# Performance work log

Measured on AMD Instinct MI355X. Metric: run time of the kernel, lower is better.

Reference implementation:

```python
import jax, jax.numpy as jnp
import numpy as np

K = 1024  # codebook size
D = 256   # embedding dim


def setup_inputs() -> dict:
    key = jax.random.key(0)
    k1, k2 = jax.random.split(key)
    z_e_x = jax.random.normal(k1, (32, D, 32, 32), dtype=jnp.float32)  # NCHW
    # nn.Embedding weight initialized uniform(-1/K, 1/K)
    W = jax.random.uniform(k2, (K, D), dtype=jnp.float32, minval=-1.0 / K, maxval=1.0 / K)
    return {"z_e_x": z_e_x, "W": W}


def reference(z_e_x, W):
    # permute NCHW -> NHWC, flatten spatial, nearest-codebook lookup (vq)
    z = jnp.transpose(z_e_x, (0, 2, 3, 1))            # [B, H, Wd, D]
    B, H, Wd, Dd = z.shape
    flat = z.reshape(-1, Dd)                           # [N, D]
    # squared L2 distances: ||z||^2 - 2 z.W^T + ||W||^2
    z_sq = jnp.sum(flat * flat, axis=1, keepdims=True)         # [N, 1]
    w_sq = jnp.sum(W * W, axis=1)                               # [K]
    dists = z_sq - 2.0 * (flat @ W.T) + w_sq[None, :]           # [N, K]
    idx = jnp.argmin(dists, axis=1)                             # [N]
    latents = idx.reshape(B, H, Wd)                             # [B, H, Wd] int indices
    return latents
```

## Files before the change

### kernel.cpp

```cpp
#include <hip/hip_runtime.h>

#define NPOS 32768
#define DDIM 256
#define KCODES 1024

typedef __attribute__((ext_vector_type(8))) short bf16x8;
typedef __attribute__((ext_vector_type(4))) float f32x4;
typedef unsigned long long u64;

__device__ __forceinline__ float sqr_rn(float x) {
    float r = x * x;
    asm volatile("" : "+v"(r));
    return r;
}
__device__ __forceinline__ float add_rn(float a, float b) {
    float r = a + b;
    asm volatile("" : "+v"(r));
    return r;
}

__device__ __forceinline__ unsigned short f2bf(float x) {
    unsigned u = __float_as_uint(x);
    return (unsigned short)((u + 0x7fffu + ((u >> 16) & 1u)) >> 16);
}

__device__ __forceinline__ u64 packm(float s, int code) {
    unsigned b = __float_as_uint(s);
    unsigned mm = ((unsigned)((int)b >> 31)) | 0x80000000u;
    return ((u64)(b ^ mm) << 32) | (unsigned)code;
}

__global__ __launch_bounds__(256) void wprep(const float* __restrict__ W,
                                             float* __restrict__ wsq,
                                             unsigned short* __restrict__ wb16t) {
    const int t   = threadIdx.x;
    const int bid = blockIdx.x;
    const int row = bid * 16 + (t >> 4);
    const int j   = t & 15;
    const float* base = W + row * DDIM + (j & 7) + (j >> 3) * 128;
    float r = sqr_rn(base[0]);
#pragma unroll
    for (int i = 1; i < 16; ++i) r = add_rn(r, sqr_rn(base[i * 8]));
#pragma unroll
    for (int m = 1; m <= 8; m <<= 1) r = add_rn(r, __shfl_xor(r, m));
    if (j == 0) wsq[row] = r;
#pragma unroll
    for (int jj = 0; jj < 2; ++jj) {
        const int u  = t + jj * 256;
        const int n  = bid * 16 + (u >> 5);
        const int k8 = u & 31;
        const float4 f0 = *(const float4*)&W[n * DDIM + k8 * 8];
        const float4 f1 = *(const float4*)&W[n * DDIM + k8 * 8 + 4];
        bf16x8 o;
        o[0] = (short)f2bf(f0.x); o[1] = (short)f2bf(f0.y);
        o[2] = (short)f2bf(f0.z); o[3] = (short)f2bf(f0.w);
        o[4] = (short)f2bf(f1.x); o[5] = (short)f2bf(f1.y);
        o[6] = (short)f2bf(f1.z); o[7] = (short)f2bf(f1.w);
        const int kk = k8 >> 2, kq = k8 & 3;
        *(bf16x8*)&wb16t[(n >> 8) * 65536 + kk * 8192 + kq * 2048 + (n & 255) * 8] = o;
    }
}

#define ZS 260
__global__ __launch_bounds__(256)
void vq_fused(const float* __restrict__ z,
              const float* __restrict__ W,
              const float* __restrict__ wsq,
              const unsigned short* __restrict__ wb16t,
              int* __restrict__ out) {
    union Sm {
        unsigned short At[8192];
        float          Zs[32 * ZS];
    };
    __shared__ Sm  sm;
    __shared__ u64 redL[32 * 8];

    const int t   = threadIdx.x;
    const int bid = blockIdx.x;
    const int img = bid >> 5;
    const int p0  = (bid & 31) * 32;

    {
        const float* zbase = z + img * (DDIM * 1024) + p0;
#pragma unroll
        for (int jj = 0; jj < 4; ++jj) {
            const int u_ = t + jj * 256;
            const int m  = u_ & 31;
            const int k8 = u_ >> 5;
            const float* src = zbase + k8 * 8192 + m;
            bf16x8 o;
#pragma unroll
            for (int e = 0; e < 8; ++e) o[e] = (short)f2bf(src[e * 1024]);
            *(bf16x8*)&sm.At[k8 * 256 + m * 8] = o;
        }
    }
    __syncthreads();

    const int w  = t >> 6;
    const int l  = t & 63;
    const int ln = l & 15;
    const int q  = l >> 4;
    const int nw = w * 64;

    const char* aBase = (const char*)sm.At + q * 512 + ln * 16;
    const char* bBase = (const char*)wb16t + q * 4096 + (nw + ln) * 16;

    float s0[2][4], s1[2][4];
    int   i0[2][4], i1[2][4];
#pragma unroll
    for (int mf = 0; mf < 2; ++mf)
#pragma unroll
        for (int reg = 0; reg < 4; ++reg) {
            s0[mf][reg] = 1e30f; s1[mf][reg] = 1e30f;
            i0[mf][reg] = 0;     i1[mf][reg] = 0;
        }

#pragma unroll 1
    for (int nblk = 0; nblk < 4; ++nblk) {
        const int n0 = nblk * 256;
        float wq[4];
#pragma unroll
        for (int nf = 0; nf < 4; ++nf) wq[nf] = wsq[n0 + nw + nf * 16 + ln];

        f32x4 acc[2][4];
#pragma unroll
        for (int a = 0; a < 2; ++a)
#pragma unroll
            for (int b = 0; b < 4; ++b) acc[a][b] = (f32x4)(0.f);

        const char* bP = bBase + nblk * 131072;
        bf16x8 bfr[4], bnx[4];
#pragma unroll
        for (int nf = 0; nf < 4; ++nf) bfr[nf] = *(const bf16x8*)(bP + nf * 256);

#pragma unroll 1
        for (int kk = 0; kk < 8; ++kk) {
            if (kk < 7) {
#pragma unroll
                for (int nf = 0; nf < 4; ++nf)
                    bnx[nf] = *(const bf16x8*)(bP + (kk + 1) * 16384 + nf * 256);
            }
            bf16x8 afr[2];
#pragma unroll
            for (int mf = 0; mf < 2; ++mf)
                afr[mf] = *(const bf16x8*)(aBase + kk * 2048 + mf * 256);
#pragma unroll
            for (int nf = 0; nf < 4; ++nf)
#pragma unroll
                for (int mf = 0; mf < 2; ++mf)
                    acc[mf][nf] = __builtin_amdgcn_mfma_f32_16x16x32_bf16(
                        afr[mf], bfr[nf], acc[mf][nf], 0, 0, 0);
#pragma unroll
            for (int nf = 0; nf < 4; ++nf) bfr[nf] = bnx[nf];
        }

#pragma unroll
        for (int mf = 0; mf < 2; ++mf) {
#pragma unroll
            for (int reg = 0; reg < 4; ++reg) {
#pragma unroll
                for (int nf = 0; nf < 4; ++nf) {
                    const float s  = fmaf(-2.f, acc[mf][nf][reg], wq[nf]);
                    const int   cc = n0 + nw + nf * 16 + ln;
                    if (s < s0[mf][reg]) {
                        s1[mf][reg] = s0[mf][reg]; i1[mf][reg] = i0[mf][reg];
                        s0[mf][reg] = s;           i0[mf][reg] = cc;
                    } else if (s < s1[mf][reg]) {
                        s1[mf][reg] = s;           i1[mf][reg] = cc;
                    }
                }
            }
        }
    }

#pragma unroll
    for (int mf = 0; mf < 2; ++mf) {
#pragma unroll
        for (int reg = 0; reg < 4; ++reg) {
            const int row = mf * 16 + q * 4 + reg;
            u64 c0 = packm(s0[mf][reg], i0[mf][reg]);
            u64 c1 = packm(s1[mf][reg], i1[mf][reg]);
#pragma unroll
            for (int m = 1; m <= 8; m <<= 1) {
                const u64 o0 = __shfl_xor(c0, m);
                const u64 o1 = __shfl_xor(c1, m);
                const u64 hi = (c0 < o0) ? o0 : c0;
                c0 = (c0 < o0) ? c0 : o0;
                const u64 lo = (c1 < o1) ? c1 : o1;
                c1 = (hi < lo) ? hi : lo;
            }
            if (ln == 0) {
                redL[row * 8 + w * 2]     = c0;
                redL[row * 8 + w * 2 + 1] = c1;
            }
        }
    }
    __syncthreads();

    const float* zimg = z + img * (DDIM * 1024) + p0;
#pragma unroll
    for (int jj = 0; jj < 8; ++jj) {
        const int f4 = t + jj * 256;
        const int d = f4 >> 3, p4 = f4 & 7;
        const float4 v = *(const float4*)&zimg[d * 1024 + p4 * 4];
        sm.Zs[(p4 * 4 + 0) * ZS + d] = v.x;
        sm.Zs[(p4 * 4 + 1) * ZS + d] = v.y;
        sm.Zs[(p4 * 4 + 2) * ZS + d] = v.z;
        sm.Zs[(p4 * 4 + 3) * ZS + d] = v.w;
    }
    __syncthreads();
    {
        const int pl = t >> 3, slot = t & 7;
        const float* zr = &sm.Zs[pl * ZS];

        float h0 = sqr_rn(zr[slot]);
        float h1 = sqr_rn(zr[128 + slot]);
#pragma unroll
        for (int i = 1; i < 16; ++i) {
            h0 = add_rn(h0, sqr_rn(zr[slot + 8 * i]));
            h1 = add_rn(h1, sqr_rn(zr[128 + slot + 8 * i]));
        }
#pragma unroll
        for (int m = 1; m <= 4; m <<= 1) {
            h0 = add_rn(h0, __shfl_xor(h0, m));
            h1 = add_rn(h1, __shfl_xor(h1, m));
        }
        const float zq = add_rn(h0, h1);

        const int code = (int)(unsigned)(redL[pl * 8 + slot] & 0xffffffffULL);
        const float* wr = W + code * DDIM;
        float M = 0.f;
#pragma unroll 8
        for (int d4 = 0; d4 < 64; ++d4) {
            const float4 zv = *(const float4*)&zr[d4 * 4];
            const float4 wv = *(const float4*)&wr[d4 * 4];
            M = fmaf(zv.x, wv.x, M);
            M = fmaf(zv.y, wv.y, M);
            M = fmaf(zv.z, wv.z, M);
            M = fmaf(zv.w, wv.w, M);
        }
        const float s = add_rn(fmaf(-2.f, M, zq), wsq[code]);
        u64 v = ((u64)__float_as_uint(s) << 32) | (unsigned)code;
#pragma unroll
        for (int m = 1; m <= 4; m <<= 1) {
            const u64 o = __shfl_xor(v, m);
            if (o < v) v = o;
        }
        if (slot == 0) out[img * 1024 + p0 + pl] = (int)(unsigned)(v & 0xffffffffULL);
    }
}

extern "C" void kernel_launch(void* const* d_in, const int* in_sizes, int n_in,
                              void* d_out, int out_size, void* d_ws, size_t ws_size,
                              hipStream_t stream) {
    const float* z = (const float*)d_in[0];
    const float* W = (const float*)d_in[1];
    int* out = (int*)d_out;

    char* ws = (char*)d_ws;
    float*          wsq   = (float*)ws;
    unsigned short* wb16t = (unsigned short*)(ws + 4096);

    wprep<<<KCODES / 16, 256, 0, stream>>>(W, wsq, wb16t);
    vq_fused<<<NPOS / 32, 256, 0, stream>>>(z, W, wsq, wb16t, out);
}
```

Baseline: 149.2 us.

## Halve rescoring LDS buffer, unroll B double-buffer by two, add occupancy hint

Shrinks the fp32 Z staging union from 32 to 16 rows, so the exact-rescoring epilogue now runs in two passes of 16 positions, with only half the threads active each pass. The B-fragment prefetch becomes a manually unrolled ping-pong (bA/bB), which removes the register copy at the end of each k step. A min-waves hint of 6 is added to launch_bounds. Together these aim to lower LDS and register use so more blocks fit per CU, at the cost of extra barriers and a serialized epilogue.

```diff
diff --git a/kernel.cpp b/kernel.cpp
--- a/kernel.cpp
+++ b/kernel.cpp
@@ -62,7 +62,7 @@
 }
 
 #define ZS 260
-__global__ __launch_bounds__(256)
+__global__ __launch_bounds__(256, 6)
 void vq_fused(const float* __restrict__ z,
               const float* __restrict__ W,
               const float* __restrict__ wsq,
@@ -70,7 +70,7 @@
               int* __restrict__ out) {
     union Sm {
         unsigned short At[8192];
-        float          Zs[32 * ZS];
+        float          Zs[16 * ZS];
     };
     __shared__ Sm  sm;
     __shared__ u64 redL[32 * 8];
@@ -129,29 +129,45 @@
             for (int b = 0; b < 4; ++b) acc[a][b] = (f32x4)(0.f);
 
         const char* bP = bBase + nblk * 131072;
-        bf16x8 bfr[4], bnx[4];
-#pragma unroll
-        for (int nf = 0; nf < 4; ++nf) bfr[nf] = *(const bf16x8*)(bP + nf * 256);
+        bf16x8 bA[4], bB[4];
+#pragma unroll
+        for (int nf = 0; nf < 4; ++nf) bA[nf] = *(const bf16x8*)(bP + nf * 256);
 
 #pragma unroll 1
-        for (int kk = 0; kk < 8; ++kk) {
-            if (kk < 7) {
+        for (int kk2 = 0; kk2 < 4; ++kk2) {
+            const int kkE = kk2 * 2;
+#pragma unroll
+            for (int nf = 0; nf < 4; ++nf)
+                bB[nf] = *(const bf16x8*)(bP + (kkE + 1) * 16384 + nf * 256);
+            {
+                bf16x8 afr[2];
+#pragma unroll
+                for (int mf = 0; mf < 2; ++mf)
+                    afr[mf] = *(const bf16x8*)(aBase + kkE * 2048 + mf * 256);
 #pragma unroll
                 for (int nf = 0; nf < 4; ++nf)
-                    bnx[nf] = *(const bf16x8*)(bP + (kk + 1) * 16384 + nf * 256);
-            }
-            bf16x8 afr[2];
-#pragma unroll
-            for (int mf = 0; mf < 2; ++mf)
-                afr[mf] = *(const bf16x8*)(aBase + kk * 2048 + mf * 256);
-#pragma unroll
-            for (int nf = 0; nf < 4; ++nf)
+#pragma unroll
+                    for (int mf = 0; mf < 2; ++mf)
+                        acc[mf][nf] = __builtin_amdgcn_mfma_f32_16x16x32_bf16(
+                            afr[mf], bA[nf], acc[mf][nf], 0, 0, 0);
+            }
+            if (kk2 < 3) {
+#pragma unroll
+                for (int nf = 0; nf < 4; ++nf)
+                    bA[nf] = *(const bf16x8*)(bP + (kkE + 2) * 16384 + nf * 256);
+            }
+            {
+                bf16x8 afr[2];
 #pragma unroll
                 for (int mf = 0; mf < 2; ++mf)
-                    acc[mf][nf] = __builtin_amdgcn_mfma_f32_16x16x32_bf16(
-                        afr[mf], bfr[nf], acc[mf][nf], 0, 0, 0);
-#pragma unroll
-            for (int nf = 0; nf < 4; ++nf) bfr[nf] = bnx[nf];
+                    afr[mf] = *(const bf16x8*)(aBase + (kkE + 1) * 2048 + mf * 256);
+#pragma unroll
+                for (int nf = 0; nf < 4; ++nf)
+#pragma unroll
+                    for (int mf = 0; mf < 2; ++mf)
+                        acc[mf][nf] = __builtin_amdgcn_mfma_f32_16x16x32_bf16(
+                            afr[mf], bB[nf], acc[mf][nf], 0, 0, 0);
+            }
         }
 
 #pragma unroll
@@ -198,55 +214,60 @@
     __syncthreads();
 
     const float* zimg = z + img * (DDIM * 1024) + p0;
-#pragma unroll
-    for (int jj = 0; jj < 8; ++jj) {
-        const int f4 = t + jj * 256;
-        const int d = f4 >> 3, p4 = f4 & 7;
-        const float4 v = *(const float4*)&zimg[d * 1024 + p4 * 4];
-        sm.Zs[(p4 * 4 + 0) * ZS + d] = v.x;
-        sm.Zs[(p4 * 4 + 1) * ZS + d] = v.y;
-        sm.Zs[(p4 * 4 + 2) * ZS + d] = v.z;
-        sm.Zs[(p4 * 4 + 3) * ZS + d] = v.w;
-    }
-    __syncthreads();
-    {
-        const int pl = t >> 3, slot = t & 7;
-        const float* zr = &sm.Zs[pl * ZS];
-
-        float h0 = sqr_rn(zr[slot]);
-        float h1 = sqr_rn(zr[128 + slot]);
-#pragma unroll
-        for (int i = 1; i < 16; ++i) {
-            h0 = add_rn(h0, sqr_rn(zr[slot + 8 * i]));
-            h1 = add_rn(h1, sqr_rn(zr[128 + slot + 8 * i]));
-        }
-#pragma unroll
-        for (int m = 1; m <= 4; m <<= 1) {
-            h0 = add_rn(h0, __shfl_xor(h0, m));
-            h1 = add_rn(h1, __shfl_xor(h1, m));
-        }
-        const float zq = add_rn(h0, h1);
-
-        const int code = (int)(unsigned)(redL[pl * 8 + slot] & 0xffffffffULL);
-        const float* wr = W + code * DDIM;
-        float M = 0.f;
+#pragma unroll 1
+    for (int c = 0; c < 2; ++c) {
+#pragma unroll
+        for (int jj = 0; jj < 4; ++jj) {
+            const int f4 = t + jj * 256;
+            const int d  = f4 >> 2;
+            const int p4 = f4 & 3;
+            const float4 v = *(const float4*)&zimg[d * 1024 + c * 16 + p4 * 4];
+            sm.Zs[(p4 * 4 + 0) * ZS + d] = v.x;
+            sm.Zs[(p4 * 4 + 1) * ZS + d] = v.y;
+            sm.Zs[(p4 * 4 + 2) * ZS + d] = v.z;
+            sm.Zs[(p4 * 4 + 3) * ZS + d] = v.w;
+        }
+        __syncthreads();
+        if (t < 128) {
+            const int pl = t >> 3, slot = t & 7;
+            const float* zr = &sm.Zs[pl * ZS];
+
+            float h0 = sqr_rn(zr[slot]);
+            float h1 = sqr_rn(zr[128 + slot]);
+#pragma unroll
+            for (int i = 1; i < 16; ++i) {
+                h0 = add_rn(h0, sqr_rn(zr[slot + 8 * i]));
+                h1 = add_rn(h1, sqr_rn(zr[128 + slot + 8 * i]));
+            }
+#pragma unroll
+            for (int m = 1; m <= 4; m <<= 1) {
+                h0 = add_rn(h0, __shfl_xor(h0, m));
+                h1 = add_rn(h1, __shfl_xor(h1, m));
+            }
+            const float zq = add_rn(h0, h1);
+
+            const int code = (int)(unsigned)(redL[(c * 16 + pl) * 8 + slot] & 0xffffffffULL);
+            const float* wr = W + code * DDIM;
+            float M = 0.f;
 #pragma unroll 8
-        for (int d4 = 0; d4 < 64; ++d4) {
-            const float4 zv = *(const float4*)&zr[d4 * 4];
-            const float4 wv = *(const float4*)&wr[d4 * 4];
-            M = fmaf(zv.x, wv.x, M);
-            M = fmaf(zv.y, wv.y, M);
-            M = fmaf(zv.z, wv.z, M);
-            M = fmaf(zv.w, wv.w, M);
-        }
-        const float s = add_rn(fmaf(-2.f, M, zq), wsq[code]);
-        u64 v = ((u64)__float_as_uint(s) << 32) | (unsigned)code;
-#pragma unroll
-        for (int m = 1; m <= 4; m <<= 1) {
-            const u64 o = __shfl_xor(v, m);
-            if (o < v) v = o;
-        }
-        if (slot == 0) out[img * 1024 + p0 + pl] = (int)(unsigned)(v & 0xffffffffULL);
+            for (int d4 = 0; d4 < 64; ++d4) {
+                const float4 zv = *(const float4*)&zr[d4 * 4];
+                const float4 wv = *(const float4*)&wr[d4 * 4];
+                M = fmaf(zv.x, wv.x, M);
+                M = fmaf(zv.y, wv.y, M);
+                M = fmaf(zv.z, wv.z, M);
+                M = fmaf(zv.w, wv.w, M);
+            }
+            const float s = add_rn(fmaf(-2.f, M, zq), wsq[code]);
+            u64 v = ((u64)__float_as_uint(s) << 32) | (unsigned)code;
+#pragma unroll
+            for (int m = 1; m <= 4; m <<= 1) {
+                const u64 o = __shfl_xor(v, m);
+                if (o < v) v = o;
+            }
+            if (slot == 0) out[img * 1024 + p0 + c * 16 + pl] = (int)(unsigned)(v & 0xffffffffULL);
+        }
+        __syncthreads();
     }
 }
 
```

Result: slower. 178.9 us (+19.9%).
